# Performance work log

Measured on AMD Instinct MI355X. Metric: run time of the kernel, lower is better.

The kernel has to match this reference:

```python
import math
import jax, jax.numpy as jnp
import numpy as np

H = 12  # n_heads
NEG = -1e9

def setup_inputs() -> dict:
    key = jax.random.key(0)
    ks = jax.random.split(key, 5)
    B, S, D = 1, 4096, 768
    x = jax.random.normal(ks[0], (B, S, D), dtype=jnp.float32)
    Wqkv = jax.random.normal(ks[1], (D, 3 * D), dtype=jnp.float32) * (1.0 / math.sqrt(D))
    bqkv = jnp.zeros((3 * D,), dtype=jnp.float32)
    Wout = jax.random.normal(ks[2], (D, D), dtype=jnp.float32) * (1.0 / math.sqrt(D))
    bout = jnp.zeros((D,), dtype=jnp.float32)
    rel_bias = jax.random.normal(ks[3], (H, S, S), dtype=jnp.float32) * 0.02
    # additive causal mask: 0 on/below diagonal, large negative above
    causal_mask = jnp.where(jnp.tril(jnp.ones((S, S), dtype=bool)), 0.0, NEG).astype(jnp.float32)
    return {"x": x, "Wqkv": Wqkv, "bqkv": bqkv, "Wout": Wout, "bout": bout,
            "rel_bias": rel_bias, "causal_mask": causal_mask}

def reference(x, Wqkv, bqkv, Wout, bout, rel_bias, causal_mask):
    B, S, D = x.shape
    hd = D // H
    qkv = x @ Wqkv + bqkv                      # [B,S,3D]
    q, k, v = jnp.split(qkv, 3, axis=-1)
    def heads(t):  # [B,S,D] -> [B,H,S,hd]
        return t.reshape(B, S, H, hd).transpose(0, 2, 1, 3)
    q, k, v = heads(q), heads(k), heads(v)
    scores = jnp.einsum('bhqd,bhkd->bhqk', q, k) / math.sqrt(hd)
    scores = scores + rel_bias[None] + causal_mask[None, None]
    attn = jax.nn.softmax(scores, axis=-1)     # dropout p=0.0 -> identity
    out = jnp.einsum('bhqk,bhkd->bhqd', attn, v)
    out = out.transpose(0, 2, 1, 3).reshape(B, S, D)
    return out @ Wout + bout
```

## Files before the change

kernel.cpp:

```cpp
#include <hip/hip_runtime.h>
#include <stdint.h>

typedef _Float16 f16;
typedef _Float16 f16x8 __attribute__((ext_vector_type(8)));
typedef _Float16 f16x4 __attribute__((ext_vector_type(4)));
typedef float f32x4 __attribute__((ext_vector_type(4)));

#define NEGF -1e30f

static __device__ __forceinline__ f32x4 mfma16(f16x8 a, f16x8 b, f32x4 c) {
    return __builtin_amdgcn_mfma_f32_16x16x32_f16(a, b, c, 0, 0, 0);
}

static __device__ __forceinline__ void gload_lds16(const void* g, void* l) {
    __builtin_amdgcn_global_load_lds(
        (const __attribute__((address_space(1))) unsigned int*)g,
        (__attribute__((address_space(3))) unsigned int*)l, 16, 0, 0);
}

__global__ void cast_f32_f16(const float* __restrict__ src, f16* __restrict__ dst, int n) {
    int idx = blockIdx.x * blockDim.x + threadIdx.x;
    int stride = gridDim.x * blockDim.x;
    for (int i = idx * 4; i < n; i += stride * 4) {
        float4 v = *(const float4*)(src + i);
        f16x4 h;
        h[0] = (f16)v.x; h[1] = (f16)v.y; h[2] = (f16)v.z; h[3] = (f16)v.w;
        *(f16x4*)(dst + i) = h;
    }
}

__global__ void transpose_cast(const float* __restrict__ src, f16* __restrict__ dst, int R, int C) {
    __shared__ float tile[32][33];
    const int c0 = blockIdx.x * 32, r0 = blockIdx.y * 32;
    const int tx = threadIdx.x & 31, ty = threadIdx.x >> 5;
#pragma unroll
    for (int i = 0; i < 32; i += 8)
        tile[ty + i][tx] = src[(size_t)(r0 + ty + i) * C + c0 + tx];
    __syncthreads();
#pragma unroll
    for (int i = 0; i < 32; i += 8)
        dst[(size_t)(c0 + ty + i) * R + r0 + tx] = (f16)tile[tx][ty + i];
}

__global__ void __launch_bounds__(256, 2)
gemm_qkv(const f16* __restrict__ A, const f16* __restrict__ Bt,
         const float* __restrict__ bias,
         f16* __restrict__ Qb, f16* __restrict__ Kb, f16* __restrict__ Vtb, int K) {
    __shared__ alignas(16) f16 As[2][128 * 32];
    __shared__ alignas(16) f16 Bs[2][128 * 32];
    const int t = threadIdx.x;
    const int lane = t & 63, wid = t >> 6;
    const int wm = wid >> 1, wn = wid & 1;
    const int lr = lane & 15, lg = lane >> 4;
    const int m0 = blockIdx.y * 128, n0 = blockIdx.x * 128;

    auto stage = [&](int buf, int k0) {
#pragma unroll
        for (int i = 0; i < 2; i++) {
            const int cc = t + i * 256;
            const int rr = cc >> 2, ch = cc & 3;
            gload_lds16(A + (size_t)(m0 + rr) * K + k0 + ch * 8, (f16*)As[buf] + cc * 8);
            gload_lds16(Bt + (size_t)(n0 + rr) * K + k0 + ch * 8, (f16*)Bs[buf] + cc * 8);
        }
    };

    f32x4 acc[4][4] = {};
    stage(0, 0);
    __syncthreads();
    const int NK = K / 32;
    for (int it = 0; it < NK; ++it) {
        const int cur = it & 1;
        if (it + 1 < NK) stage(cur ^ 1, (it + 1) * 32);
        f16x8 af[4], bf[4];
#pragma unroll
        for (int i = 0; i < 4; i++)
            af[i] = *(const f16x8*)((f16*)As[cur] + (wm * 64 + i * 16 + lr) * 32 + lg * 8);
#pragma unroll
        for (int j = 0; j < 4; j++)
            bf[j] = *(const f16x8*)((f16*)Bs[cur] + (wn * 64 + j * 16 + lr) * 32 + lg * 8);
#pragma unroll
        for (int i = 0; i < 4; i++)
#pragma unroll
            for (int j = 0; j < 4; j++)
                acc[i][j] = mfma16(af[i], bf[j], acc[i][j]);
        __syncthreads();
    }
#pragma unroll
    for (int i = 0; i < 4; i++) {
#pragma unroll
        for (int j = 0; j < 4; j++) {
            const int n_g = n0 + wn * 64 + j * 16 + lr;
            const float bv = bias[n_g];
#pragma unroll
            for (int jj = 0; jj < 4; jj++) {
                const int m_g = m0 + wm * 64 + i * 16 + lg * 4 + jj;
                const float val = acc[i][j][jj] + bv;
                if (n_g < 768) {
                    Qb[(((n_g >> 6) * 4096) + m_g) * 64 + (n_g & 63)] = (f16)(val * 0.125f);
                } else if (n_g < 1536) {
                    const int n2 = n_g - 768;
                    Kb[(((n2 >> 6) * 4096) + m_g) * 64 + (n2 & 63)] = (f16)val;
                } else {
                    const int n2 = n_g - 1536;
                    Vtb[((n2 >> 6) * 64 + (n2 & 63)) * 4096 + m_g] = (f16)val;
                }
            }
        }
    }
}

__global__ void __launch_bounds__(256, 3)
gemm_out(const f16* __restrict__ A, const f16* __restrict__ Bt,
         const float* __restrict__ bias, float* __restrict__ Cout, int K, int N) {
    __shared__ alignas(16) f16 As[2][128 * 32];
    __shared__ alignas(16) f16 Bs[2][64 * 32];
    const int t = threadIdx.x;
    const int lane = t & 63, wid = t >> 6;
    const int lr = lane & 15, lg = lane >> 4;
    const int m0 = blockIdx.y * 128, n0 = blockIdx.x * 64;

    auto stage = [&](int buf, int k0) {
#pragma unroll
        for (int i = 0; i < 2; i++) {
            const int cc = t + i * 256;
            const int rr = cc >> 2, ch = cc & 3;
            gload_lds16(A + (size_t)(m0 + rr) * K + k0 + ch * 8, (f16*)As[buf] + cc * 8);
        }
        const int rr = t >> 2, ch = t & 3;
        gload_lds16(Bt + (size_t)(n0 + rr) * K + k0 + ch * 8, (f16*)Bs[buf] + t * 8);
    };

    f32x4 acc[2][4] = {};
    stage(0, 0);
    __syncthreads();
    const int NK = K / 32;
    for (int it = 0; it < NK; ++it) {
        const int cur = it & 1;
        if (it + 1 < NK) stage(cur ^ 1, (it + 1) * 32);
        f16x8 af[2], bf[4];
#pragma unroll
        for (int i = 0; i < 2; i++)
            af[i] = *(const f16x8*)((f16*)As[cur] + (wid * 32 + i * 16 + lr) * 32 + lg * 8);
#pragma unroll
        for (int j = 0; j < 4; j++)
            bf[j] = *(const f16x8*)((f16*)Bs[cur] + (j * 16 + lr) * 32 + lg * 8);
#pragma unroll
        for (int i = 0; i < 2; i++)
#pragma unroll
            for (int j = 0; j < 4; j++)
                acc[i][j] = mfma16(af[i], bf[j], acc[i][j]);
        __syncthreads();
    }
#pragma unroll
    for (int i = 0; i < 2; i++) {
#pragma unroll
        for (int j = 0; j < 4; j++) {
            const int n_g = n0 + j * 16 + lr;
            const float bv = bias[n_g];
#pragma unroll
            for (int jj = 0; jj < 4; jj++) {
                const int m_g = m0 + wid * 32 + i * 16 + lg * 4 + jj;
                Cout[(size_t)m_g * N + n_g] = acc[i][j][jj] + bv;
            }
        }
    }
}

__global__ void __launch_bounds__(256, 3)
attn_fwd(const f16* __restrict__ Qb, const f16* __restrict__ Kb,
         const f16* __restrict__ Vtb, const float* __restrict__ rel_bias,
         f16* __restrict__ Opart, float* __restrict__ mpart, float* __restrict__ lpart) {
    __shared__ alignas(16) f16 Ks[2][64 * 64];
    __shared__ alignas(16) f16 Vs[2][64 * 64];
    __shared__ alignas(16) f16 Ps[4][32 * 72];
    const int bid = blockIdx.x;
    const int h = bid / 144;
    int rr = bid % 144;
    int qb = 0;
    for (;;) { const int n = (qb + 4) >> 2; if (rr < n) break; rr -= n; ++qb; }
    const int c = rr;
    const int lo = c * 8;
    const int hi = min(lo + 8, 2 * qb + 2);

    const int t = threadIdx.x, lane = t & 63, wid = t >> 6;
    const int lr = lane & 15, lg = lane >> 4;
    const int g = qb * 4 + wid;
    const int q0w = g * 32;
    const int ktd = g >> 1;
    const f16* Qh = Qb + (size_t)h * 4096 * 64;
    const f16* Kh = Kb + (size_t)h * 4096 * 64;
    const f16* Vh = Vtb + (size_t)h * 64 * 4096;
    const float* rbh = rel_bias + (size_t)h * 4096 * 4096;

    auto stage = [&](int buf, int kt) {
        const int kbase = kt * 64;
#pragma unroll
        for (int i = 0; i < 2; i++) {
            const int cc = t + i * 256;
            const int row = cc >> 3;
            const int cswz = (((cc & 7) * 16) ^ ((row & 7) << 4)) >> 1;
            gload_lds16(Kh + (size_t)(kbase + row) * 64 + cswz, (f16*)Ks[buf] + cc * 8);
            gload_lds16(Vh + (size_t)row * 4096 + kbase + cswz, (f16*)Vs[buf] + cc * 8);
        }
    };

    f16x8 qf[2][2];
#pragma unroll
    for (int nf = 0; nf < 2; nf++)
#pragma unroll
        for (int kd = 0; kd < 2; kd++)
            qf[nf][kd] = *(const f16x8*)(Qh + (size_t)(q0w + nf * 16 + lr) * 64 + kd * 32 + lg * 8);

    f32x4 o[2][4] = {};
    float mrow[2] = {NEGF, NEGF};
    float lrow[2] = {0.f, 0.f};
    float4 rb[2][4];
    auto biasPrefetch = [&](int kt) {
#pragma unroll
        for (int nf = 0; nf < 2; nf++)
#pragma unroll
            for (int mf = 0; mf < 4; mf++)
                rb[nf][mf] = *(const float4*)(rbh + (size_t)(q0w + nf * 16 + lr) * 4096 + kt * 64 + mf * 16 + lg * 4);
    };
    const float L2E = 1.4426950408889634f;

    stage(0, lo);
    if (lo <= ktd) {
        biasPrefetch(lo);
        asm volatile("s_waitcnt vmcnt(8)" ::: "memory");
    } else {
        asm volatile("s_waitcnt vmcnt(0)" ::: "memory");
    }
    __builtin_amdgcn_s_barrier();
    asm volatile("" ::: "memory");

    for (int kt = lo; kt < hi; kt++) {
        const int kbase = kt * 64;
        const int cur = (kt - lo) & 1;
        if (kt + 1 < hi) stage(cur ^ 1, kt + 1);
        const bool nextBias = (kt + 1 <= ktd) && (kt + 1 < hi);
        if (kt <= ktd) {
            f32x4 st[4][2] = {};
#pragma unroll
            for (int kd = 0; kd < 2; kd++) {
#pragma unroll
                for (int mf = 0; mf < 4; mf++) {
                    const int r = mf * 16 + lr;
                    const int cf = ((kd * 64 + lg * 16) ^ ((r & 7) << 4)) >> 1;
                    const f16x8 kf = *(const f16x8*)((f16*)Ks[cur] + r * 64 + cf);
#pragma unroll
                    for (int nf = 0; nf < 2; nf++)
                        st[mf][nf] = mfma16(kf, qf[nf][kd], st[mf][nf]);
                }
            }
            const bool diag = (kt == ktd);
            float fs2[2];
#pragma unroll
            for (int nf = 0; nf < 2; nf++) {
                const int q_g = q0w + nf * 16 + lr;
                float mx = NEGF;
#pragma unroll
                for (int mf = 0; mf < 4; mf++) {
                    const float rbv[4] = {rb[nf][mf].x, rb[nf][mf].y, rb[nf][mf].z, rb[nf][mf].w};
#pragma unroll
                    for (int jj = 0; jj < 4; jj++) {
                        float v = st[mf][nf][jj] + rbv[jj];
                        if (diag) {
                            const int k_g = kbase + mf * 16 + lg * 4 + jj;
                            v = (k_g > q_g) ? NEGF : v;
                        }
                        st[mf][nf][jj] = v;
                        mx = fmaxf(mx, v);
                    }
                }
                mx = fmaxf(mx, __shfl_xor(mx, 16));
                mx = fmaxf(mx, __shfl_xor(mx, 32));
                const float mnew = fmaxf(mrow[nf], mx);
                const float m2 = mnew * L2E;
                fs2[nf] = exp2f(mrow[nf] * L2E - m2);
                mrow[nf] = mnew;
                float rsum = 0.f;
#pragma unroll
                for (int mf = 0; mf < 4; mf++) {
                    f16x4 pv;
#pragma unroll
                    for (int jj = 0; jj < 4; jj++) {
                        const float p = exp2f(__builtin_fmaf(st[mf][nf][jj], L2E, -m2));
                        rsum += p;
                        pv[jj] = (f16)p;
                    }
                    *(f16x4*)(&Ps[wid][(nf * 16 + lr) * 72 + mf * 16 + lg * 4]) = pv;
                }
                rsum += __shfl_xor(rsum, 16);
                rsum += __shfl_xor(rsum, 32);
                lrow[nf] = lrow[nf] * fs2[nf] + rsum;
            }
            if (nextBias) biasPrefetch(kt + 1);
#pragma unroll
            for (int qf2 = 0; qf2 < 2; qf2++) {
#pragma unroll
                for (int jj = 0; jj < 4; jj++) {
                    const float f = __shfl(fs2[qf2], lg * 4 + jj);
#pragma unroll
                    for (int df = 0; df < 4; df++)
                        o[qf2][df][jj] *= f;
                }
            }
#pragma unroll
            for (int kk = 0; kk < 2; kk++) {
                f16x8 pa[2], vb[4];
#pragma unroll
                for (int qf2 = 0; qf2 < 2; qf2++)
                    pa[qf2] = *(const f16x8*)(&Ps[wid][(qf2 * 16 + lr) * 72 + kk * 32 + lg * 8]);
#pragma unroll
                for (int df = 0; df < 4; df++) {
                    const int r = df * 16 + lr;
                    const int cf = ((kk * 64 + lg * 16) ^ ((r & 7) << 4)) >> 1;
                    vb[df] = *(const f16x8*)((f16*)Vs[cur] + r * 64 + cf);
                }
#pragma unroll
                for (int qf2 = 0; qf2 < 2; qf2++)
#pragma unroll
                    for (int df = 0; df < 4; df++)
                        o[qf2][df] = mfma16(pa[qf2], vb[df], o[qf2][df]);
            }
        }
        if (nextBias) asm volatile("s_waitcnt vmcnt(8)" ::: "memory");
        else          asm volatile("s_waitcnt vmcnt(0)" ::: "memory");
        __builtin_amdgcn_s_barrier();
        asm volatile("" ::: "memory");
    }

    const int s = (h * 128 + g) * 8 + c;
    f16* Op = Opart + (size_t)s * 2048;
#pragma unroll
    for (int qf2 = 0; qf2 < 2; qf2++)
#pragma unroll
        for (int df = 0; df < 4; df++)
#pragma unroll
            for (int jj = 0; jj < 4; jj++)
                Op[(qf2 * 16 + lg * 4 + jj) * 64 + df * 16 + lr] = (f16)o[qf2][df][jj];
    if (lg == 0) {
#pragma unroll
        for (int nf = 0; nf < 2; nf++) {
            mpart[(size_t)s * 32 + nf * 16 + lr] = mrow[nf];
            lpart[(size_t)s * 32 + nf * 16 + lr] = lrow[nf];
        }
    }
}

__global__ void __launch_bounds__(256)
merge_norm(const f16* __restrict__ Opart, const float* __restrict__ mpart,
           const float* __restrict__ lpart, f16* __restrict__ Ob) {
    __shared__ float wls[8][32];
    __shared__ float Linv[32];
    const int g = blockIdx.x, h = blockIdx.y;
    const int nc = (g >> 4) + 1;
    const size_t sb = (size_t)(h * 128 + g) * 8;
    const int t = threadIdx.x;
    if (t < 32) {
        float M = NEGF;
#pragma unroll
        for (int i = 0; i < 8; i++)
            if (i < nc) M = fmaxf(M, mpart[(sb + i) * 32 + t]);
        float L = 0.f;
#pragma unroll
        for (int i = 0; i < 8; i++)
            if (i < nc) {
                const float w = __expf(mpart[(sb + i) * 32 + t] - M);
                wls[i][t] = w;
                L += w * lpart[(sb + i) * 32 + t];
            }
        Linv[t] = 1.f / L;
    }
    __syncthreads();
    const int row = t >> 3, dq = t & 7;
    float acc[8] = {};
#pragma unroll
    for (int i = 0; i < 8; i++) {
        if (i < nc) {
            const f16x8 a = *(const f16x8*)(Opart + (sb + i) * 2048 + row * 64 + dq * 8);
            const float w = wls[i][row];
#pragma unroll
            for (int j = 0; j < 8; j++) acc[j] += w * (float)a[j];
        }
    }
    const float inv = Linv[row];
    const int q = g * 32 + row;
    f16x8 ov;
#pragma unroll
    for (int j = 0; j < 8; j++) ov[j] = (f16)(acc[j] * inv);
    *(f16x8*)(Ob + (size_t)q * 768 + h * 64 + dq * 8) = ov;
}

extern "C" void kernel_launch(void* const* d_in, const int* in_sizes, int n_in,
                              void* d_out, int out_size, void* d_ws, size_t ws_size,
                              hipStream_t stream) {
    const float* x = (const float*)d_in[0];
    const float* Wqkv = (const float*)d_in[1];
    const float* bqkv = (const float*)d_in[2];
    const float* Wout = (const float*)d_in[3];
    const float* bout = (const float*)d_in[4];
    const float* rel_bias = (const float*)d_in[5];
    float* out = (float*)d_out;

    f16* p = (f16*)d_ws;
    f16* xb = p;     p += (size_t)4096 * 768;
    f16* WqkvT = p;  p += (size_t)2304 * 768;
    f16* WoutT = p;  p += (size_t)768 * 768;
    f16* Qb = p;     p += (size_t)12 * 4096 * 64;
    f16* Kb = p;     p += (size_t)12 * 4096 * 64;
    f16* Vtb = p;    p += (size_t)12 * 4096 * 64;
    f16* Ob = p;     p += (size_t)4096 * 768;
    f16* Opart = p;  p += (size_t)12 * 128 * 8 * 2048;
    float* fp = (float*)p;
    float* mpart = fp;  fp += (size_t)12 * 128 * 8 * 32;
    float* lpart = fp;  fp += (size_t)12 * 128 * 8 * 32;

    cast_f32_f16<<<3072, 256, 0, stream>>>(x, xb, 4096 * 768);
    transpose_cast<<<dim3(2304 / 32, 768 / 32), 256, 0, stream>>>(Wqkv, WqkvT, 768, 2304);
    transpose_cast<<<dim3(768 / 32, 768 / 32), 256, 0, stream>>>(Wout, WoutT, 768, 768);
    gemm_qkv<<<dim3(18, 32), 256, 0, stream>>>(xb, WqkvT, bqkv, Qb, Kb, Vtb, 768);
    attn_fwd<<<dim3(1728), 256, 0, stream>>>(Qb, Kb, Vtb, rel_bias, Opart, mpart, lpart);
    merge_norm<<<dim3(128, 12), 256, 0, stream>>>(Opart, mpart, lpart, Ob);
    gemm_out<<<dim3(12, 32), 256, 0, stream>>>(Ob, WoutT, bout, out, 768, 768);
}
```

Measured before the change: 236.2 us.

## Load K/V fragments directly from global memory and drop LDS double-buffering

Removes the shared-memory K and V double buffers, the async global-to-LDS staging and the per-tile block barriers. Each wave now reads its K and V MFMA fragments straight from global memory (relying on L1/L2 for reuse across the four waves) and stops at its own diagonal tile instead of iterating to the block's upper bound. The rel_bias prefetch that overlapped with compute is also gone; bias is loaded at the top of each tile. This lets waves proceed independently without barrier stalls, at the cost of redundant global traffic and exposed load latency with no software pipelining.

```diff
diff --git a/kernel.cpp b/kernel.cpp
--- a/kernel.cpp
+++ b/kernel.cpp
@@ -170,8 +170,6 @@
 attn_fwd(const f16* __restrict__ Qb, const f16* __restrict__ Kb,
          const f16* __restrict__ Vtb, const float* __restrict__ rel_bias,
          f16* __restrict__ Opart, float* __restrict__ mpart, float* __restrict__ lpart) {
-    __shared__ alignas(16) f16 Ks[2][64 * 64];
-    __shared__ alignas(16) f16 Vs[2][64 * 64];
     __shared__ alignas(16) f16 Ps[4][32 * 72];
     const int bid = blockIdx.x;
     const int h = bid / 144;
@@ -187,23 +185,12 @@
     const int g = qb * 4 + wid;
     const int q0w = g * 32;
     const int ktd = g >> 1;
+    const int myhi = min(hi, ktd + 1);
     const f16* Qh = Qb + (size_t)h * 4096 * 64;
     const f16* Kh = Kb + (size_t)h * 4096 * 64;
     const f16* Vh = Vtb + (size_t)h * 64 * 4096;
     const float* rbh = rel_bias + (size_t)h * 4096 * 4096;
 
-    auto stage = [&](int buf, int kt) {
-        const int kbase = kt * 64;
-#pragma unroll
-        for (int i = 0; i < 2; i++) {
-            const int cc = t + i * 256;
-            const int row = cc >> 3;
-            const int cswz = (((cc & 7) * 16) ^ ((row & 7) << 4)) >> 1;
-            gload_lds16(Kh + (size_t)(kbase + row) * 64 + cswz, (f16*)Ks[buf] + cc * 8);
-            gload_lds16(Vh + (size_t)row * 4096 + kbase + cswz, (f16*)Vs[buf] + cc * 8);
-        }
-    };
-
     f16x8 qf[2][2];
 #pragma unroll
     for (int nf = 0; nf < 2; nf++)
@@ -214,121 +201,94 @@
     f32x4 o[2][4] = {};
     float mrow[2] = {NEGF, NEGF};
     float lrow[2] = {0.f, 0.f};
-    float4 rb[2][4];
-    auto biasPrefetch = [&](int kt) {
+    const float L2E = 1.4426950408889634f;
+
+    for (int kt = lo; kt < myhi; kt++) {
+        const int kbase = kt * 64;
+        float4 rb[2][4];
 #pragma unroll
         for (int nf = 0; nf < 2; nf++)
 #pragma unroll
             for (int mf = 0; mf < 4; mf++)
-                rb[nf][mf] = *(const float4*)(rbh + (size_t)(q0w + nf * 16 + lr) * 4096 + kt * 64 + mf * 16 + lg * 4);
-    };
-    const float L2E = 1.4426950408889634f;
-
-    stage(0, lo);
-    if (lo <= ktd) {
-        biasPrefetch(lo);
-        asm volatile("s_waitcnt vmcnt(8)" ::: "memory");
-    } else {
-        asm volatile("s_waitcnt vmcnt(0)" ::: "memory");
-    }
-    __builtin_amdgcn_s_barrier();
-    asm volatile("" ::: "memory");
-
-    for (int kt = lo; kt < hi; kt++) {
-        const int kbase = kt * 64;
-        const int cur = (kt - lo) & 1;
-        if (kt + 1 < hi) stage(cur ^ 1, kt + 1);
-        const bool nextBias = (kt + 1 <= ktd) && (kt + 1 < hi);
-        if (kt <= ktd) {
-            f32x4 st[4][2] = {};
-#pragma unroll
-            for (int kd = 0; kd < 2; kd++) {
-#pragma unroll
-                for (int mf = 0; mf < 4; mf++) {
-                    const int r = mf * 16 + lr;
-                    const int cf = ((kd * 64 + lg * 16) ^ ((r & 7) << 4)) >> 1;
-                    const f16x8 kf = *(const f16x8*)((f16*)Ks[cur] + r * 64 + cf);
-#pragma unroll
-                    for (int nf = 0; nf < 2; nf++)
-                        st[mf][nf] = mfma16(kf, qf[nf][kd], st[mf][nf]);
+                rb[nf][mf] = *(const float4*)(rbh + (size_t)(q0w + nf * 16 + lr) * 4096 + kbase + mf * 16 + lg * 4);
+        f32x4 st[4][2] = {};
+#pragma unroll
+        for (int kd = 0; kd < 2; kd++) {
+#pragma unroll
+            for (int mf = 0; mf < 4; mf++) {
+                const f16x8 kf = *(const f16x8*)(Kh + (size_t)(kbase + mf * 16 + lr) * 64 + kd * 32 + lg * 8);
+#pragma unroll
+                for (int nf = 0; nf < 2; nf++)
+                    st[mf][nf] = mfma16(kf, qf[nf][kd], st[mf][nf]);
+            }
+        }
+        const bool diag = (kt == ktd);
+        float fs2[2];
+#pragma unroll
+        for (int nf = 0; nf < 2; nf++) {
+            const int q_g = q0w + nf * 16 + lr;
+            float mx = NEGF;
+#pragma unroll
+            for (int mf = 0; mf < 4; mf++) {
+                const float rbv[4] = {rb[nf][mf].x, rb[nf][mf].y, rb[nf][mf].z, rb[nf][mf].w};
+#pragma unroll
+                for (int jj = 0; jj < 4; jj++) {
+                    float v = st[mf][nf][jj] + rbv[jj];
+                    if (diag) {
+                        const int k_g = kbase + mf * 16 + lg * 4 + jj;
+                        v = (k_g > q_g) ? NEGF : v;
+                    }
+                    st[mf][nf][jj] = v;
+                    mx = fmaxf(mx, v);
                 }
             }
-            const bool diag = (kt == ktd);
-            float fs2[2];
-#pragma unroll
-            for (int nf = 0; nf < 2; nf++) {
-                const int q_g = q0w + nf * 16 + lr;
-                float mx = NEGF;
-#pragma unroll
-                for (int mf = 0; mf < 4; mf++) {
-                    const float rbv[4] = {rb[nf][mf].x, rb[nf][mf].y, rb[nf][mf].z, rb[nf][mf].w};
-#pragma unroll
-                    for (int jj = 0; jj < 4; jj++) {
-                        float v = st[mf][nf][jj] + rbv[jj];
-                        if (diag) {
-                            const int k_g = kbase + mf * 16 + lg * 4 + jj;
-                            v = (k_g > q_g) ? NEGF : v;
-                        }
-                        st[mf][nf][jj] = v;
-                        mx = fmaxf(mx, v);
-                    }
+            mx = fmaxf(mx, __shfl_xor(mx, 16));
+            mx = fmaxf(mx, __shfl_xor(mx, 32));
+            const float mnew = fmaxf(mrow[nf], mx);
+            const float m2 = mnew * L2E;
+            fs2[nf] = exp2f(mrow[nf] * L2E - m2);
+            mrow[nf] = mnew;
+            float rsum = 0.f;
+#pragma unroll
+            for (int mf = 0; mf < 4; mf++) {
+                f16x4 pv;
+#pragma unroll
+                for (int jj = 0; jj < 4; jj++) {
+                    const float p = exp2f(__builtin_fmaf(st[mf][nf][jj], L2E, -m2));
+                    rsum += p;
+                    pv[jj] = (f16)p;
                 }
-                mx = fmaxf(mx, __shfl_xor(mx, 16));
-                mx = fmaxf(mx, __shfl_xor(mx, 32));
-                const float mnew = fmaxf(mrow[nf], mx);
-                const float m2 = mnew * L2E;
-                fs2[nf] = exp2f(mrow[nf] * L2E - m2);
-                mrow[nf] = mnew;
-                float rsum = 0.f;
-#pragma unroll
-                for (int mf = 0; mf < 4; mf++) {
-                    f16x4 pv;
-#pragma unroll
-                    for (int jj = 0; jj < 4; jj++) {
-                        const float p = exp2f(__builtin_fmaf(st[mf][nf][jj], L2E, -m2));
-                        rsum += p;
-                        pv[jj] = (f16)p;
-                    }
-                    *(f16x4*)(&Ps[wid][(nf * 16 + lr) * 72 + mf * 16 + lg * 4]) = pv;
-                }
-                rsum += __shfl_xor(rsum, 16);
-                rsum += __shfl_xor(rsum, 32);
-                lrow[nf] = lrow[nf] * fs2[nf] + rsum;
-            }
-            if (nextBias) biasPrefetch(kt + 1);
-#pragma unroll
-            for (int qf2 = 0; qf2 < 2; qf2++) {
-#pragma unroll
-                for (int jj = 0; jj < 4; jj++) {
-                    const float f = __shfl(fs2[qf2], lg * 4 + jj);
-#pragma unroll
-                    for (int df = 0; df < 4; df++)
-                        o[qf2][df][jj] *= f;
-                }
-            }
-#pragma unroll
-            for (int kk = 0; kk < 2; kk++) {
-                f16x8 pa[2], vb[4];
+                *(f16x4*)(&Ps[wid][(nf * 16 + lr) * 72 + mf * 16 + lg * 4]) = pv;
+            }
+            rsum += __shfl_xor(rsum, 16);
+            rsum += __shfl_xor(rsum, 32);
+            lrow[nf] = lrow[nf] * fs2[nf] + rsum;
+        }
+        asm volatile("s_waitcnt lgkmcnt(0)" ::: "memory");
+#pragma unroll
+        for (int qf2 = 0; qf2 < 2; qf2++) {
+#pragma unroll
+            for (int jj = 0; jj < 4; jj++) {
+                const float f = __shfl(fs2[qf2], lg * 4 + jj);
+#pragma unroll
+                for (int df = 0; df < 4; df++)
+                    o[qf2][df][jj] *= f;
+            }
+        }
+#pragma unroll
+        for (int kk = 0; kk < 2; kk++) {
+            f16x8 pa[2];
+#pragma unroll
+            for (int qf2 = 0; qf2 < 2; qf2++)
+                pa[qf2] = *(const f16x8*)(&Ps[wid][(qf2 * 16 + lr) * 72 + kk * 32 + lg * 8]);
+#pragma unroll
+            for (int df = 0; df < 4; df++) {
+                const f16x8 vb = *(const f16x8*)(Vh + (size_t)(df * 16 + lr) * 4096 + kbase + kk * 32 + lg * 8);
 #pragma unroll
                 for (int qf2 = 0; qf2 < 2; qf2++)
-                    pa[qf2] = *(const f16x8*)(&Ps[wid][(qf2 * 16 + lr) * 72 + kk * 32 + lg * 8]);
-#pragma unroll
-                for (int df = 0; df < 4; df++) {
-                    const int r = df * 16 + lr;
-                    const int cf = ((kk * 64 + lg * 16) ^ ((r & 7) << 4)) >> 1;
-                    vb[df] = *(const f16x8*)((f16*)Vs[cur] + r * 64 + cf);
-                }
-#pragma unroll
-                for (int qf2 = 0; qf2 < 2; qf2++)
-#pragma unroll
-                    for (int df = 0; df < 4; df++)
-                        o[qf2][df] = mfma16(pa[qf2], vb[df], o[qf2][df]);
-            }
-        }
-        if (nextBias) asm volatile("s_waitcnt vmcnt(8)" ::: "memory");
-        else          asm volatile("s_waitcnt vmcnt(0)" ::: "memory");
-        __builtin_amdgcn_s_barrier();
-        asm volatile("" ::: "memory");
+                    o[qf2][df] = mfma16(pa[qf2], vb, o[qf2][df]);
+            }
+        }
     }
 
     const int s = (h * 128 + g) * 8 + c;
```

Result: slower. 285.9 us (+21.0%).
